# Kernel tuning notes

Measured on AMD Instinct MI355X. Metric: run time of the kernel, lower is better.

Reference implementation:

```python
import jax, jax.numpy as jnp
import numpy as np

T = 4096
V = 88   # visible_dim
H = 512  # hidden_dim
R = 512  # rnn_hidden_dim
REG_FACTOR = 0.2
GIBBS_STEPS = 20
EPS = 1e-6


def setup_inputs() -> dict:
    key = jax.random.key(0)
    ks = jax.random.split(key, 8)
    scale = 1.0 / np.sqrt(H)
    return {
        "visible": (jax.random.uniform(ks[0], (T, V)) < 0.5).astype(jnp.float32),
        "rand_h": jax.random.uniform(ks[1], (T - 1, GIBBS_STEPS, H), dtype=jnp.float32),
        "rand_v": jax.random.uniform(ks[2], (T - 1, GIBBS_STEPS, V), dtype=jnp.float32),
        "w": jax.random.normal(ks[3], (H, V), dtype=jnp.float32) * scale,
        "wuu": jax.random.normal(ks[4], (R, R), dtype=jnp.float32) * scale,
        "wuv": jax.random.normal(ks[5], (V, R), dtype=jnp.float32) * scale,
        "wuh": jax.random.normal(ks[6], (H, R), dtype=jnp.float32) * scale,
        "wvu": jax.random.normal(ks[7], (R, V), dtype=jnp.float32) * scale,
        "bv": jnp.zeros((V,), jnp.float32),
        "bh": jnp.zeros((H,), jnp.float32),
        "bu": jnp.zeros((R,), jnp.float32),
        "u0": jnp.zeros((R,), jnp.float32),
    }


def reference(visible, rand_h, rand_v, w, wuu, wuv, wuh, wvu, bv, bh, bu, u0):
    time_steps = visible.shape[0]
    v_seq = visible[1:]  # v_t for t = 1..T-1, shape [T-1, V]

    # RNN state depends only on data, not on Gibbs samples -> single scan.
    def u_step(u_prev, v_t):
        u_new = jnp.tanh(wvu @ v_t + wuu @ u_prev + bu)
        return u_new, u_prev  # emit u_{t-1} (bias conditioning state)

    _, u_prev = jax.lax.scan(u_step, u0, v_seq)  # [T-1, R]

    # Per-timestep RBM biases (F.linear(u, W, b) = u @ W.T + b).
    bh_t = u_prev @ wuh.T + bh  # [T-1, H]
    bv_t = u_prev @ wuv.T + bv  # [T-1, V]

    # 20 Gibbs steps, batched over all time steps at once.
    def gibbs_step(v, rands):
        rh, rv = rands  # [T-1, H], [T-1, V]
        p_h = jax.nn.sigmoid(v @ w.T + bh_t)
        h = jax.nn.relu(jnp.sign(p_h - rh))         # Bernoulli sample
        p_v = jax.nn.sigmoid(h @ w + bv_t)
        v_new = jax.nn.relu(jnp.sign(p_v - rv))
        return v_new, None

    neg, _ = jax.lax.scan(
        gibbs_step, v_seq,
        (jnp.swapaxes(rand_h, 0, 1), jnp.swapaxes(rand_v, 0, 1)),
    )  # negative samples [T-1, V]

    # Cross-entropy between data and sigmoid(bv_t), summed then /time_steps.
    y_t = jax.nn.sigmoid(bv_t)
    total_cost = jnp.sum(
        -v_seq * jnp.log(EPS + y_t) - (1.0 - v_seq) * jnp.log(EPS + 1.0 - y_t)
    ) / time_steps

    reg_term = (jnp.linalg.norm(wuv) + jnp.linalg.norm(wuh)) * REG_FACTOR
    total_cost = total_cost + reg_term

    mse = jnp.mean(jnp.abs(v_seq - neg), axis=1)  # per-timestep, [T-1]
    return total_cost, mse, reg_term
```

## Files before the change

### kernel.cpp

```cpp
#include <hip/hip_runtime.h>
#include <cstdint>
#include <cstddef>

#define T4096 4096
#define TM1 4095
#define NV 88
#define NH 512
#define NR 512
#define GS 20
#define EPSV 1e-6f

#define U_OFF 0
#define AB_OFF 2096640
#define BV_OFF 4193280
#define SC_OFF 4553640

__device__ __forceinline__ unsigned int agent_load_u32(const unsigned int* p) {
  return __hip_atomic_load(p, __ATOMIC_RELAXED, __HIP_MEMORY_SCOPE_AGENT);
}
__device__ __forceinline__ void agent_store_f32(float* p, float v) {
  __hip_atomic_store(p, v, __ATOMIC_RELAXED, __HIP_MEMORY_SCOPE_AGENT);
}
__device__ __forceinline__ float sigmoidf_(float x) {
  return 1.0f / (1.0f + expf(-x));
}

__device__ __forceinline__ void store_sc0(float* p, float v) {
  asm volatile("global_store_dword %0, %1, off sc0" :: "v"(p), "v"(v) : "memory");
}
__device__ __forceinline__ unsigned load_sc0(const unsigned* p) {
  unsigned r;
  asm volatile("global_load_dword %0, %1, off sc0\n\ts_waitcnt vmcnt(0)"
               : "=v"(r) : "v"(p) : "memory");
  return r;
}

__device__ __forceinline__ unsigned poll_nd_sc0(const unsigned* p,
                                                unsigned& s1, unsigned& s2,
                                                unsigned& s3, unsigned& s4) {
  unsigned rA;
  asm volatile(
    "v_mov_b32 %0, -1\n\t"
    "global_load_dword %1, %5, off sc0\n\t"
    "global_load_dword %2, %5, off sc0\n\t"
    "global_load_dword %3, %5, off sc0\n\t"
    "global_load_dword %4, %5, off sc0\n\t"
    "Lr%=:\n\t"
    "s_waitcnt vmcnt(3)\n\t"
    "v_cmp_ne_u32 vcc, -1, %1\n\t"
    "v_cndmask_b32 %0, %0, %1, vcc\n\t"
    "v_cmp_eq_u32 vcc, -1, %0\n\t"
    "s_cbranch_vccz Le%=\n\t"
    "global_load_dword %1, %5, off sc0\n\t"
    "s_waitcnt vmcnt(3)\n\t"
    "v_cmp_ne_u32 vcc, -1, %2\n\t"
    "v_cndmask_b32 %0, %0, %2, vcc\n\t"
    "v_cmp_eq_u32 vcc, -1, %0\n\t"
    "s_cbranch_vccz Le%=\n\t"
    "global_load_dword %2, %5, off sc0\n\t"
    "s_waitcnt vmcnt(3)\n\t"
    "v_cmp_ne_u32 vcc, -1, %3\n\t"
    "v_cndmask_b32 %0, %0, %3, vcc\n\t"
    "v_cmp_eq_u32 vcc, -1, %0\n\t"
    "s_cbranch_vccz Le%=\n\t"
    "global_load_dword %3, %5, off sc0\n\t"
    "s_waitcnt vmcnt(3)\n\t"
    "v_cmp_ne_u32 vcc, -1, %4\n\t"
    "v_cndmask_b32 %0, %0, %4, vcc\n\t"
    "v_cmp_eq_u32 vcc, -1, %0\n\t"
    "s_cbranch_vccz Le%=\n\t"
    "global_load_dword %4, %5, off sc0\n\t"
    "s_branch Lr%=\n\t"
    "Le%=:\n\t"
    : "=&v"(rA), "+v"(s1), "+v"(s2), "+v"(s3), "+v"(s4)
    : "v"(p) : "vcc", "memory");
  return rA;
}
__device__ __forceinline__ unsigned poll_nd_sys(const unsigned* p,
                                                unsigned& s1, unsigned& s2,
                                                unsigned& s3, unsigned& s4) {
  unsigned rA;
  asm volatile(
    "v_mov_b32 %0, -1\n\t"
    "global_load_dword %1, %5, off sc0 sc1\n\t"
    "global_load_dword %2, %5, off sc0 sc1\n\t"
    "global_load_dword %3, %5, off sc0 sc1\n\t"
    "global_load_dword %4, %5, off sc0 sc1\n\t"
    "Lq%=:\n\t"
    "s_waitcnt vmcnt(3)\n\t"
    "v_cmp_ne_u32 vcc, -1, %1\n\t"
    "v_cndmask_b32 %0, %0, %1, vcc\n\t"
    "v_cmp_eq_u32 vcc, -1, %0\n\t"
    "s_cbranch_vccz Lf%=\n\t"
    "global_load_dword %1, %5, off sc0 sc1\n\t"
    "s_waitcnt vmcnt(3)\n\t"
    "v_cmp_ne_u32 vcc, -1, %2\n\t"
    "v_cndmask_b32 %0, %0, %2, vcc\n\t"
    "v_cmp_eq_u32 vcc, -1, %0\n\t"
    "s_cbranch_vccz Lf%=\n\t"
    "global_load_dword %2, %5, off sc0 sc1\n\t"
    "s_waitcnt vmcnt(3)\n\t"
    "v_cmp_ne_u32 vcc, -1, %3\n\t"
    "v_cndmask_b32 %0, %0, %3, vcc\n\t"
    "v_cmp_eq_u32 vcc, -1, %0\n\t"
    "s_cbranch_vccz Lf%=\n\t"
    "global_load_dword %3, %5, off sc0 sc1\n\t"
    "s_waitcnt vmcnt(3)\n\t"
    "v_cmp_ne_u32 vcc, -1, %4\n\t"
    "v_cndmask_b32 %0, %0, %4, vcc\n\t"
    "v_cmp_eq_u32 vcc, -1, %0\n\t"
    "s_cbranch_vccz Lf%=\n\t"
    "global_load_dword %4, %5, off sc0 sc1\n\t"
    "s_branch Lq%=\n\t"
    "Lf%=:\n\t"
    : "=&v"(rA), "+v"(s1), "+v"(s2), "+v"(s3), "+v"(s4)
    : "v"(p) : "vcc", "memory");
  return rA;
}

__global__ __launch_bounds__(256) void k_a(const float* __restrict__ visible,
                                           const float* __restrict__ wvu,
                                           const float* __restrict__ bu,
                                           float* __restrict__ A) {
  __shared__ float vbuf[NV * 8];
  const int tid = threadIdx.x;
  const int t0 = blockIdx.x * 8;
  for (int idx = tid; idx < NV * 8; idx += 256) {
    int j = idx / NV, v = idx - j * NV;
    int t = t0 + j;
    vbuf[v * 8 + j] = (t < TM1) ? visible[(size_t)(t + 1) * NV + v] : 0.f;
  }
  __syncthreads();
  for (int rr = 0; rr < 2; rr++) {
    int r = tid + rr * 256;
    float b0 = bu[r];
    float acc[8];
#pragma unroll
    for (int j = 0; j < 8; j++) acc[j] = b0;
    const float* wr = wvu + (size_t)r * NV;
    for (int v = 0; v < NV; v++) {
      float wv = wr[v];
#pragma unroll
      for (int j = 0; j < 8; j++) acc[j] = fmaf(wv, vbuf[v * 8 + j], acc[j]);
    }
#pragma unroll
    for (int j = 0; j < 8; j++) {
      int t = t0 + j;
      if (t < TM1) A[(size_t)t * NR + r] = acc[j];
    }
  }
}

__global__ __launch_bounds__(256) void k_r(const float* __restrict__ wuv,
                                           const float* __restrict__ wuh,
                                           float* __restrict__ sc) {
  size_t stride = (size_t)gridDim.x * 256;
  size_t gid = (size_t)blockIdx.x * 256 + threadIdx.x;
  float s1 = 0.f, s2 = 0.f;
  for (size_t i = gid; i < (size_t)NV * NR; i += stride) { float x = wuv[i]; s1 = fmaf(x, x, s1); }
  for (size_t i = gid; i < (size_t)NH * NR; i += stride) { float x = wuh[i]; s2 = fmaf(x, x, s2); }
  for (int off = 32; off > 0; off >>= 1) {
    s1 += __shfl_down(s1, off, 64);
    s2 += __shfl_down(s2, off, 64);
  }
  if ((threadIdx.x & 63) == 0) {
    atomicAdd(&sc[1], s1);
    atomicAdd(&sc[2], s2);
  }
}

__global__ __launch_bounds__(512, 2) void k_u9(const float* __restrict__ wuu,
                                               const float* __restrict__ A,
                                               const float* __restrict__ u0,
                                               float* __restrict__ U,
                                               unsigned* __restrict__ ub) {
  __shared__ int s_slot;
  __shared__ int s_fast;
  __shared__ float u_buf[NR];
  __shared__ float partials[2][1024];
  const int tid = threadIdx.x;
  unsigned* claimc = ub + 8;
  unsigned* winner = ub + 16;
  unsigned* hs     = ub + 17;
  unsigned* vd     = ub + 33;

  if (tid == 0) {
    unsigned xcd;
    asm volatile("s_getreg_b32 %0, hwreg(HW_REG_XCC_ID, 0, 4)" : "=s"(xcd));
    xcd &= 7u;
    unsigned c = atomicAdd(&claimc[xcd], 1u);
    int slot = -1;
    if (c < 4u) {
      if (c == 3u) atomicCAS(winner, 0xFFFFFFFFu, xcd);
      unsigned wnr;
      do { wnr = agent_load_u32(winner); } while (wnr == 0xFFFFFFFFu);
      if (wnr == xcd) slot = (int)c;
    }
    s_slot = slot;
  }
  __syncthreads();
  const int slot = s_slot;
  if (slot < 0) return;

  if (tid == 0) {
    int fast = 1;
    for (int round = 0; round < 4 && fast; ++round) {
      unsigned* hw = hs + round * 4;
      store_sc0((float*)&hw[slot], 0.0f);
      for (int o = 0; o < 4; ++o) {
        if (o == slot) continue;
        int ok = 0;
        for (int it = 0; it < 300; ++it) {
          if (load_sc0(&hw[o]) != 0xFFFFFFFFu) { ok = 1; break; }
        }
        if (!ok) fast = 0;
      }
    }
    __hip_atomic_store(&vd[slot], (unsigned)(fast ? 1 : 0),
                       __ATOMIC_RELAXED, __HIP_MEMORY_SCOPE_AGENT);
    for (int o = 0; o < 4; ++o) {
      unsigned v;
      do { v = agent_load_u32(&vd[o]); } while (v == 0xFFFFFFFFu);
      if (v != 1u) fast = 0;
    }
    s_fast = fast;
  }
  __syncthreads();
  const int fast = s_fast;

  const int lane = tid & 63;
  const int kc   = tid >> 6;
  const int r0   = slot * 128;
  const bool is_red = (kc >> 1) == slot;
  const int s_row = ((kc & 1) << 6) + lane;
  float* ubw = u_buf + kc * 64;

  float WregA[64], WregB[64];
  {
    const float* wra = wuu + (size_t)(r0 + lane) * NR + kc * 64;
    const float* wrb = wuu + (size_t)(r0 + lane + 64) * NR + kc * 64;
#pragma unroll
    for (int i = 0; i < 16; i++) {
      ((float4*)WregA)[i] = ((const float4*)wra)[i];
      ((float4*)WregB)[i] = ((const float4*)wrb)[i];
    }
  }
#pragma unroll
  for (int i = 0; i < 64; i++) asm volatile("" : "+v"(WregA[i]));
#pragma unroll
  for (int i = 0; i < 64; i++) asm volatile("" : "+v"(WregB[i]));

  float val = 0.f, a_cur = 0.f;
  if (is_red) {
    agent_store_f32(&U[r0 + s_row], u0[r0 + s_row]);
    a_cur = A[r0 + s_row];
  }
  unsigned ps1 = 0, ps2 = 0, ps3 = 0, ps4 = 0;
  __syncthreads();

#define KU_STEP(T_, UVAL_) do {                                                \
    ubw[lane] = (UVAL_);                                                       \
    float acc0 = 0.f, acc1 = 0.f;                                              \
    _Pragma("unroll")                                                          \
    for (int i = 0; i < 64; i += 4) {                                          \
      float4 uv = *(const float4*)(ubw + i);                                   \
      acc0 = fmaf(WregA[i],     uv.x, acc0);                                   \
      acc1 = fmaf(WregB[i],     uv.x, acc1);                                   \
      acc0 = fmaf(WregA[i + 1], uv.y, acc0);                                   \
      acc1 = fmaf(WregB[i + 1], uv.y, acc1);                                   \
      acc0 = fmaf(WregA[i + 2], uv.z, acc0);                                   \
      acc1 = fmaf(WregB[i + 2], uv.z, acc1);                                   \
      acc0 = fmaf(WregA[i + 3], uv.w, acc0);                                   \
      acc1 = fmaf(WregB[i + 3], uv.w, acc1);                                   \
    }                                                                          \
    float* pb = partials[(T_) & 1];                                            \
    pb[kc * 128 + lane] = acc0;                                                \
    pb[kc * 128 + lane + 64] = acc1;                                           \
    __syncthreads();                                                           \
    if (is_red) {                                                              \
      float s = a_cur;                                                         \
      _Pragma("unroll")                                                        \
      for (int kk = 0; kk < 8; kk++) s += pb[kk * 128 + s_row];                \
      val = tanhf(s);                                                          \
      if (fast) store_sc0(&U[(size_t)(T_) * NR + r0 + s_row], val);            \
      else      agent_store_f32(&U[(size_t)(T_) * NR + r0 + s_row], val);      \
      a_cur = A[(size_t)(T_) * NR + r0 + s_row];    \
    }                                                                          \
  } while (0)

  KU_STEP(1, u0[kc * 64 + lane]);
  for (int t = 2; t <= TM1 - 1; t++) {
    float u_val;
    if (is_red) {
      u_val = val;
    } else {
      const unsigned* p = (const unsigned*)(U + (size_t)(t - 1) * NR) + kc * 64 + lane;
      unsigned w = fast ? poll_nd_sc0(p, ps1, ps2, ps3, ps4)
                        : poll_nd_sys(p, ps1, ps2, ps3, ps4);
      u_val = __uint_as_float(w);
    }
    KU_STEP(t, u_val);
  }
#undef KU_STEP
}

__global__ __launch_bounds__(256) void k_bh(const float* __restrict__ Uu,
                                            const float* __restrict__ wuh,
                                            const float* __restrict__ wuv,
                                            const float* __restrict__ bh,
                                            const float* __restrict__ bv,
                                            const float* __restrict__ visible,
                                            float* __restrict__ bht,
                                            float* __restrict__ bvt,
                                            float* __restrict__ sc) {
  __shared__ float uT[NR * 20];
  __shared__ float red[256];
  const int tid = threadIdx.x;
  const int t0 = blockIdx.x * 16;
  const int nt = min(16, TM1 - t0);
  for (int idx = tid; idx < 16 * NR; idx += 256) {
    int tt = idx >> 9, k = idx & 511;
    uT[k * 20 + tt] = (tt < nt) ? Uu[(size_t)(t0 + tt) * NR + k] : 0.f;
  }
  __syncthreads();
  const int h1 = tid, h2 = tid + 256;
  const bool hasv = tid < NV;
  float acc1[16], acc2[16], accv[16];
#pragma unroll
  for (int i = 0; i < 16; i++) acc1[i] = acc2[i] = accv[i] = 0.f;
  const float* w1p = wuh + (size_t)h1 * NR;
  const float* w2p = wuh + (size_t)h2 * NR;
  const float* wvp = wuv + (size_t)(hasv ? tid : 0) * NR;
  for (int k = 0; k < NR; k++) {
    float u16[16];
#pragma unroll
    for (int q = 0; q < 4; q++) *(float4*)(u16 + 4 * q) = *(const float4*)(uT + k * 20 + 4 * q);
    float a = w1p[k], b = w2p[k];
    float c = hasv ? wvp[k] : 0.f;
#pragma unroll
    for (int i = 0; i < 16; i++) {
      acc1[i] = fmaf(a, u16[i], acc1[i]);
      acc2[i] = fmaf(b, u16[i], acc2[i]);
      accv[i] = fmaf(c, u16[i], accv[i]);
    }
  }
  float bh1 = bh[h1], bh2 = bh[h2];
#pragma unroll
  for (int i = 0; i < 16; i++) {
    if (i < nt) {
      bht[(size_t)(t0 + i) * NH + h1] = acc1[i] + bh1;
      bht[(size_t)(t0 + i) * NH + h2] = acc2[i] + bh2;
    }
  }
  float ce = 0.f;
  if (hasv) {
    float bvv = bv[tid];
    for (int i = 0; i < nt; i++) {
      float x = accv[i] + bvv;
      bvt[(size_t)(t0 + i) * NV + tid] = x;
      float y = sigmoidf_(x);
      float vs = visible[(size_t)(t0 + i + 1) * NV + tid];
      ce += -vs * logf(EPSV + y) - (1.f - vs) * logf(EPSV + 1.f - y);
    }
  }
  red[tid] = ce;
  __syncthreads();
  for (int s = 128; s > 0; s >>= 1) {
    if (tid < s) red[tid] += red[tid + s];
    __syncthreads();
  }
  if (tid == 0) atomicAdd(&sc[0], red[0]);
}

__global__ __launch_bounds__(256) void k_g(const float* __restrict__ w,
                                           const float* __restrict__ visible,
                                           const float* __restrict__ rand_h,
                                           const float* __restrict__ rand_v,
                                           const float* __restrict__ bht,
                                           const float* __restrict__ bvt,
                                           float* __restrict__ out) {
  __shared__ float vlds[NV * 20];
  __shared__ float hlds[NH * 20];
  const int tid = threadIdx.x;
  const int t0 = blockIdx.x * 16;
  const int nt = min(16, TM1 - t0);
  for (int idx = tid; idx < NV * 16; idx += 256) {
    int j = idx / NV, v = idx - j * NV;
    vlds[v * 20 + j] = (j < nt) ? visible[(size_t)(t0 + j + 1) * NV + v] : 0.f;
  }
  for (int idx = tid; idx < NH * 20; idx += 256) hlds[idx] = 0.f;
  __syncthreads();
  const int h1 = tid, h2 = tid + 256;
  const int tg = tid >> 5, vg = tid & 31;
  const int v0 = vg * 4;
  const bool bact = vg < 22;
  for (int k = 0; k < GS; k++) {
    {
      float acc1[16], acc2[16];
#pragma unroll
      for (int i = 0; i < 16; i++) acc1[i] = acc2[i] = 0.f;
      const float* w1p = w + (size_t)h1 * NV;
      const float* w2p = w + (size_t)h2 * NV;
      for (int v = 0; v < NV; v++) {
        float vv[16];
#pragma unroll
        for (int q = 0; q < 4; q++) *(float4*)(vv + 4 * q) = *(const float4*)(vlds + v * 20 + 4 * q);
        float a = w1p[v], b = w2p[v];
#pragma unroll
        for (int i = 0; i < 16; i++) {
          acc1[i] = fmaf(a, vv[i], acc1[i]);
          acc2[i] = fmaf(b, vv[i], acc2[i]);
        }
      }
#pragma unroll
      for (int i = 0; i < 16; i++) {
        if (i < nt) {
          size_t t = (size_t)(t0 + i);
          float x1 = acc1[i] + bht[t * NH + h1];
          float x2 = acc2[i] + bht[t * NH + h2];
          float p1 = sigmoidf_(x1);
          float p2 = sigmoidf_(x2);
          float r1 = rand_h[(t * GS + k) * NH + h1];
          float r2 = rand_h[(t * GS + k) * NH + h2];
          hlds[h1 * 20 + i] = (p1 > r1) ? 1.f : 0.f;
          hlds[h2 * 20 + i] = (p2 > r2) ? 1.f : 0.f;
        }
      }
    }
    __syncthreads();
    if (bact) {
      float acc[2][4];
#pragma unroll
      for (int a = 0; a < 2; a++)
#pragma unroll
        for (int b = 0; b < 4; b++) acc[a][b] = 0.f;
#pragma unroll 4
      for (int h = 0; h < NH; h++) {
        float2 hv = *(const float2*)(hlds + h * 20 + tg * 2);
        float4 w4 = *(const float4*)(w + (size_t)h * NV + v0);
        acc[0][0] = fmaf(hv.x, w4.x, acc[0][0]);
        acc[0][1] = fmaf(hv.x, w4.y, acc[0][1]);
        acc[0][2] = fmaf(hv.x, w4.z, acc[0][2]);
        acc[0][3] = fmaf(hv.x, w4.w, acc[0][3]);
        acc[1][0] = fmaf(hv.y, w4.x, acc[1][0]);
        acc[1][1] = fmaf(hv.y, w4.y, acc[1][1]);
        acc[1][2] = fmaf(hv.y, w4.z, acc[1][2]);
        acc[1][3] = fmaf(hv.y, w4.w, acc[1][3]);
      }
#pragma unroll
      for (int a = 0; a < 2; a++) {
        int tt = tg * 2 + a;
        if (tt < nt) {
          size_t t = (size_t)(t0 + tt);
#pragma unroll
          for (int i = 0; i < 4; i++) {
            int v = v0 + i;
            float x = acc[a][i] + bvt[t * NV + v];
            float p = sigmoidf_(x);
            float r = rand_v[(t * GS + k) * NV + v];
            vlds[v * 20 + tt] = (p > r) ? 1.f : 0.f;
          }
        }
      }
    }
    __syncthreads();
  }
  if (tid < 16 && tid < nt) {
    int tt = tid;
    float s = 0.f;
    for (int v = 0; v < NV; v++) {
      float vs = visible[(size_t)(t0 + tt + 1) * NV + v];
      s += fabsf(vs - vlds[v * 20 + tt]);
    }
    out[1 + t0 + tt] = s / 88.f;
  }
}

__global__ void k_f(const float* __restrict__ sc, float* __restrict__ out) {
  float reg = 0.2f * (sqrtf(sc[1]) + sqrtf(sc[2]));
  out[0] = sc[0] / 4096.f + reg;
  out[4096] = reg;
}

extern "C" void kernel_launch(void* const* d_in, const int* in_sizes, int n_in,
                              void* d_out, int out_size, void* d_ws, size_t ws_size,
                              hipStream_t stream) {
  const float* visible = (const float*)d_in[0];
  const float* rand_h  = (const float*)d_in[1];
  const float* rand_v  = (const float*)d_in[2];
  const float* w       = (const float*)d_in[3];
  const float* wuu     = (const float*)d_in[4];
  const float* wuv     = (const float*)d_in[5];
  const float* wuh     = (const float*)d_in[6];
  const float* wvu     = (const float*)d_in[7];
  const float* bv      = (const float*)d_in[8];
  const float* bh      = (const float*)d_in[9];
  const float* bu      = (const float*)d_in[10];
  const float* u0      = (const float*)d_in[11];
  float* out = (float*)d_out;
  float* ws = (float*)d_ws;

  float* Uarr = ws + U_OFF;
  float* Aarr = ws + AB_OFF;
  float* bht  = ws + AB_OFF;
  float* bvt  = ws + BV_OFF;
  float* sc   = ws + SC_OFF;
  unsigned* ub = (unsigned*)sc;

  hipMemsetAsync(Uarr, 0xFF, (size_t)TM1 * NR * sizeof(float), stream);
  hipMemsetAsync(sc, 0, 64, stream);
  hipMemsetAsync((char*)sc + 64, 0xFF, 96, stream);

  k_a<<<512, 256, 0, stream>>>(visible, wvu, bu, Aarr);
  k_r<<<64, 256, 0, stream>>>(wuv, wuh, sc);
  k_u9<<<64, 512, 0, stream>>>(wuu, Aarr, u0, Uarr, ub);
  k_bh<<<256, 256, 0, stream>>>(Uarr, wuh, wuv, bh, bv, visible, bht, bvt, sc);
  k_g<<<256, 256, 0, stream>>>(w, visible, rand_h, rand_v, bht, bvt, out);
  k_f<<<1, 1, 0, stream>>>(sc, out);
}
```

Before: 5.512 ms.

## Fuse bias and Gibbs stages into recurrence kernel as flag-gated consumer blocks

The serial RNN recurrence kernel now runs alongside 256 consumer blocks in the same launch. Each consumer waits on per-slice progress flags that the recurrence blocks publish every 16 steps, then computes the per-timestep biases, the cross-entropy term and the 20 Gibbs steps for 8 timesteps at a time, keeping the biases in LDS. This overlaps the dependent bias and Gibbs work with the long sequential recurrence and removes the global bht/bvt round trip and two kernel launches. The cost is system-scope stores and loads, spin-wait polling, smaller per-block tiles, and reliance on all 260 blocks being co-resident to avoid deadlock.

```diff
diff --git a/kernel.cpp b/kernel.cpp
--- a/kernel.cpp
+++ b/kernel.cpp
@@ -33,6 +33,24 @@
   asm volatile("global_load_dword %0, %1, off sc0\n\ts_waitcnt vmcnt(0)"
                : "=v"(r) : "v"(p) : "memory");
   return r;
+}
+__device__ __forceinline__ void store_sys_f32(float* p, float v) {
+  asm volatile("global_store_dword %0, %1, off sc0 sc1" :: "v"(p), "v"(v) : "memory");
+}
+__device__ __forceinline__ void store_sys_u32(unsigned* p, unsigned v) {
+  asm volatile("global_store_dword %0, %1, off sc0 sc1" :: "v"(p), "v"(v) : "memory");
+}
+__device__ __forceinline__ unsigned load_sys_u32(const unsigned* p) {
+  unsigned r;
+  asm volatile("global_load_dword %0, %1, off sc0 sc1\n\ts_waitcnt vmcnt(0)"
+               : "=v"(r) : "v"(p) : "memory");
+  return r;
+}
+__device__ __forceinline__ float load_sys_f32(const float* p) {
+  unsigned r;
+  asm volatile("global_load_dword %0, %1, off sc0 sc1\n\ts_waitcnt vmcnt(0)"
+               : "=v"(r) : "v"(p) : "memory");
+  return __uint_as_float(r);
 }
 
 __device__ __forceinline__ unsigned poll_nd_sc0(const unsigned* p,
@@ -169,20 +187,35 @@
   }
 }
 
-__global__ __launch_bounds__(512, 2) void k_u9(const float* __restrict__ wuu,
-                                               const float* __restrict__ A,
-                                               const float* __restrict__ u0,
-                                               float* __restrict__ U,
-                                               unsigned* __restrict__ ub) {
+__global__ __launch_bounds__(512, 2) void k_u11(const float* __restrict__ wuu,
+                                                float* A,
+                                                const float* __restrict__ u0,
+                                                float* __restrict__ U,
+                                                unsigned* __restrict__ ub,
+                                                const float* __restrict__ visible,
+                                                const float* __restrict__ w,
+                                                const float* __restrict__ rand_h,
+                                                const float* __restrict__ rand_v,
+                                                const float* __restrict__ wuh,
+                                                const float* __restrict__ wuv,
+                                                const float* __restrict__ bh,
+                                                const float* __restrict__ bv,
+                                                float* __restrict__ out) {
   __shared__ int s_slot;
   __shared__ int s_fast;
-  __shared__ float u_buf[NR];
-  __shared__ float partials[2][1024];
+  __shared__ int s_cid;
+  __shared__ float red2[256];
+  __shared__ __align__(16) union {
+    struct { float u_buf[NR]; float partials[2][1024]; } p;
+    struct { float bht[8 * NH]; float bvt[8 * NV]; float uT[NR * 10]; } b;
+    struct { float bht[8 * NH]; float bvt[8 * NV]; float vlds[NV * 10]; float hlds[NH * 10]; } g;
+  } sh;
   const int tid = threadIdx.x;
   unsigned* claimc = ub + 8;
   unsigned* winner = ub + 16;
   unsigned* hs     = ub + 17;
   unsigned* vd     = ub + 33;
+  unsigned* flags  = ub + 40;
 
   if (tid == 0) {
     unsigned xcd;
@@ -200,7 +233,149 @@
   }
   __syncthreads();
   const int slot = s_slot;
-  if (slot < 0) return;
+
+  if (slot < 0) {
+    if (tid == 0) s_cid = (int)atomicAdd(&ub[48], 1u);
+    __syncthreads();
+    const int cid = s_cid;
+    if (cid >= 256) return;
+    float ce = 0.f;
+    for (int half = 0; half < 2; half++) {
+      const int c = cid * 2 + half;
+      const int t0 = c * 8;
+      const int nt = min(8, TM1 - t0);
+      unsigned need = (unsigned)((t0 + nt - 1 + 15) & ~15);
+      if (need > 4080u) need = 4095u;
+      if (tid == 0) {
+        for (;;) {
+          unsigned mn = 0xFFFFFFFFu;
+          for (int i = 0; i < 8; i++) { unsigned f = load_sys_u32(&flags[i]); if (f < mn) mn = f; }
+          if (mn >= need) break;
+          __builtin_amdgcn_s_sleep(32);
+        }
+      }
+      __syncthreads();
+      for (int idx = tid; idx < 8 * NR; idx += 512) {
+        int tt = idx >> 9, k = idx & 511;
+        int t = t0 + tt;
+        float v = 0.f;
+        if (tt < nt) v = (t == 0) ? u0[k] : load_sys_f32(&A[(size_t)(t - 1) * NR + k]);
+        sh.b.uT[k * 10 + tt] = v;
+      }
+      __syncthreads();
+      {
+        const int h = tid;
+        const bool hasv = tid < NV;
+        float acc1[8], accv[8];
+#pragma unroll
+        for (int i = 0; i < 8; i++) acc1[i] = accv[i] = 0.f;
+        const float* w1p = wuh + (size_t)h * NR;
+        const float* wvp = wuv + (size_t)(hasv ? tid : 0) * NR;
+        for (int k = 0; k < NR; k++) {
+          float u8[8];
+#pragma unroll
+          for (int q = 0; q < 2; q++) *(float4*)(u8 + 4 * q) = *(const float4*)(sh.b.uT + k * 10 + 4 * q);
+          float a = w1p[k];
+          float cc = hasv ? wvp[k] : 0.f;
+#pragma unroll
+          for (int i = 0; i < 8; i++) {
+            acc1[i] = fmaf(a, u8[i], acc1[i]);
+            accv[i] = fmaf(cc, u8[i], accv[i]);
+          }
+        }
+        float bh1 = bh[h];
+#pragma unroll
+        for (int i = 0; i < 8; i++)
+          if (i < nt) sh.b.bht[i * NH + h] = acc1[i] + bh1;
+        if (hasv) {
+          float bvv = bv[tid];
+          for (int i = 0; i < nt; i++) {
+            float x = accv[i] + bvv;
+            sh.b.bvt[i * NV + tid] = x;
+            float y = sigmoidf_(x);
+            float vs = visible[(size_t)(t0 + i + 1) * NV + tid];
+            ce += -vs * logf(EPSV + y) - (1.f - vs) * logf(EPSV + 1.f - y);
+          }
+        }
+      }
+      __syncthreads();
+      for (int idx = tid; idx < NV * 8; idx += 512) {
+        int j = idx / NV, v = idx - j * NV;
+        sh.g.vlds[v * 10 + j] = (j < nt) ? visible[(size_t)(t0 + j + 1) * NV + v] : 0.f;
+      }
+      __syncthreads();
+      const int h1 = tid;
+      const int tg = tid >> 5, vg = tid & 31;
+      const int v0 = vg * 4;
+      const bool bact = (vg < 22) && (tg < 8);
+      for (int k = 0; k < GS; k++) {
+        {
+          float acc1[8];
+#pragma unroll
+          for (int i = 0; i < 8; i++) acc1[i] = 0.f;
+          const float* w1p = w + (size_t)h1 * NV;
+          for (int v = 0; v < NV; v++) {
+            float vv[8];
+#pragma unroll
+            for (int q = 0; q < 2; q++) *(float4*)(vv + 4 * q) = *(const float4*)(sh.g.vlds + v * 10 + 4 * q);
+            float a = w1p[v];
+#pragma unroll
+            for (int i = 0; i < 8; i++) acc1[i] = fmaf(a, vv[i], acc1[i]);
+          }
+#pragma unroll
+          for (int i = 0; i < 8; i++) {
+            if (i < nt) {
+              size_t t = (size_t)(t0 + i);
+              float x1 = acc1[i] + sh.g.bht[i * NH + h1];
+              float p1 = sigmoidf_(x1);
+              float r1 = rand_h[(t * GS + k) * NH + h1];
+              sh.g.hlds[h1 * 10 + i] = (p1 > r1) ? 1.f : 0.f;
+            }
+          }
+        }
+        __syncthreads();
+        if (bact && tg < nt) {
+          float acc[4] = {0.f, 0.f, 0.f, 0.f};
+#pragma unroll 4
+          for (int h = 0; h < NH; h++) {
+            float hv = sh.g.hlds[h * 10 + tg];
+            float4 w4 = *(const float4*)(w + (size_t)h * NV + v0);
+            acc[0] = fmaf(hv, w4.x, acc[0]);
+            acc[1] = fmaf(hv, w4.y, acc[1]);
+            acc[2] = fmaf(hv, w4.z, acc[2]);
+            acc[3] = fmaf(hv, w4.w, acc[3]);
+          }
+          size_t t = (size_t)(t0 + tg);
+#pragma unroll
+          for (int i = 0; i < 4; i++) {
+            int v = v0 + i;
+            float x = acc[i] + sh.g.bvt[tg * NV + v];
+            float p = sigmoidf_(x);
+            float r = rand_v[(t * GS + k) * NV + v];
+            sh.g.vlds[v * 10 + tg] = (p > r) ? 1.f : 0.f;
+          }
+        }
+        __syncthreads();
+      }
+      if (tid < nt) {
+        float s = 0.f;
+        for (int v = 0; v < NV; v++) {
+          float vs = visible[(size_t)(t0 + tid + 1) * NV + v];
+          s += fabsf(vs - sh.g.vlds[v * 10 + tid]);
+        }
+        out[1 + t0 + tid] = s / 88.f;
+      }
+      __syncthreads();
+    }
+    if (tid < 256) red2[tid] = ce;
+    __syncthreads();
+    for (int s = 128; s > 0; s >>= 1) {
+      if (tid < s) red2[tid] += red2[tid + s];
+      __syncthreads();
+    }
+    if (tid == 0) atomicAdd((float*)ub, red2[0]);
+    return;
+  }
 
   if (tid == 0) {
     int fast = 1;
@@ -233,7 +408,8 @@
   const int r0   = slot * 128;
   const bool is_red = (kc >> 1) == slot;
   const int s_row = ((kc & 1) << 6) + lane;
-  float* ubw = u_buf + kc * 64;
+  const int fid = slot * 2 + (kc & 1);
+  float* ubw = sh.p.u_buf + kc * 64;
 
   float WregA[64], WregB[64];
   {
@@ -273,7 +449,7 @@
       acc0 = fmaf(WregA[i + 3], uv.w, acc0);                                   \
       acc1 = fmaf(WregB[i + 3], uv.w, acc1);                                   \
     }                                                                          \
-    float* pb = partials[(T_) & 1];                                            \
+    float* pb = sh.p.partials[(T_) & 1];                                       \
     pb[kc * 128 + lane] = acc0;                                                \
     pb[kc * 128 + lane + 64] = acc1;                                           \
     __syncthreads();                                                           \
@@ -284,7 +460,12 @@
       val = tanhf(s);                                                          \
       if (fast) store_sc0(&U[(size_t)(T_) * NR + r0 + s_row], val);            \
       else      agent_store_f32(&U[(size_t)(T_) * NR + r0 + s_row], val);      \
+      store_sys_f32(&A[(size_t)((T_) - 1) * NR + r0 + s_row], val);            \
       a_cur = A[(size_t)(T_) * NR + r0 + s_row];    \
+      if (((T_) & 15) == 0) {                                                  \
+        asm volatile("s_waitcnt vmcnt(0)" ::: "memory");                       \
+        if (lane == 0) store_sys_u32(&flags[fid], (unsigned)(T_));             \
+      }                                                                        \
     }                                                                          \
   } while (0)
 
@@ -295,184 +476,16 @@
       u_val = val;
     } else {
       const unsigned* p = (const unsigned*)(U + (size_t)(t - 1) * NR) + kc * 64 + lane;
-      unsigned w = fast ? poll_nd_sc0(p, ps1, ps2, ps3, ps4)
-                        : poll_nd_sys(p, ps1, ps2, ps3, ps4);
-      u_val = __uint_as_float(w);
+      unsigned wv = fast ? poll_nd_sc0(p, ps1, ps2, ps3, ps4)
+                         : poll_nd_sys(p, ps1, ps2, ps3, ps4);
+      u_val = __uint_as_float(wv);
     }
     KU_STEP(t, u_val);
   }
 #undef KU_STEP
-}
-
-__global__ __launch_bounds__(256) void k_bh(const float* __restrict__ Uu,
-                                            const float* __restrict__ wuh,
-                                            const float* __restrict__ wuv,
-                                            const float* __restrict__ bh,
-                                            const float* __restrict__ bv,
-                                            const float* __restrict__ visible,
-                                            float* __restrict__ bht,
-                                            float* __restrict__ bvt,
-                                            float* __restrict__ sc) {
-  __shared__ float uT[NR * 20];
-  __shared__ float red[256];
-  const int tid = threadIdx.x;
-  const int t0 = blockIdx.x * 16;
-  const int nt = min(16, TM1 - t0);
-  for (int idx = tid; idx < 16 * NR; idx += 256) {
-    int tt = idx >> 9, k = idx & 511;
-    uT[k * 20 + tt] = (tt < nt) ? Uu[(size_t)(t0 + tt) * NR + k] : 0.f;
-  }
-  __syncthreads();
-  const int h1 = tid, h2 = tid + 256;
-  const bool hasv = tid < NV;
-  float acc1[16], acc2[16], accv[16];
-#pragma unroll
-  for (int i = 0; i < 16; i++) acc1[i] = acc2[i] = accv[i] = 0.f;
-  const float* w1p = wuh + (size_t)h1 * NR;
-  const float* w2p = wuh + (size_t)h2 * NR;
-  const float* wvp = wuv + (size_t)(hasv ? tid : 0) * NR;
-  for (int k = 0; k < NR; k++) {
-    float u16[16];
-#pragma unroll
-    for (int q = 0; q < 4; q++) *(float4*)(u16 + 4 * q) = *(const float4*)(uT + k * 20 + 4 * q);
-    float a = w1p[k], b = w2p[k];
-    float c = hasv ? wvp[k] : 0.f;
-#pragma unroll
-    for (int i = 0; i < 16; i++) {
-      acc1[i] = fmaf(a, u16[i], acc1[i]);
-      acc2[i] = fmaf(b, u16[i], acc2[i]);
-      accv[i] = fmaf(c, u16[i], accv[i]);
-    }
-  }
-  float bh1 = bh[h1], bh2 = bh[h2];
-#pragma unroll
-  for (int i = 0; i < 16; i++) {
-    if (i < nt) {
-      bht[(size_t)(t0 + i) * NH + h1] = acc1[i] + bh1;
-      bht[(size_t)(t0 + i) * NH + h2] = acc2[i] + bh2;
-    }
-  }
-  float ce = 0.f;
-  if (hasv) {
-    float bvv = bv[tid];
-    for (int i = 0; i < nt; i++) {
-      float x = accv[i] + bvv;
-      bvt[(size_t)(t0 + i) * NV + tid] = x;
-      float y = sigmoidf_(x);
-      float vs = visible[(size_t)(t0 + i + 1) * NV + tid];
-      ce += -vs * logf(EPSV + y) - (1.f - vs) * logf(EPSV + 1.f - y);
-    }
-  }
-  red[tid] = ce;
-  __syncthreads();
-  for (int s = 128; s > 0; s >>= 1) {
-    if (tid < s) red[tid] += red[tid + s];
-    __syncthreads();
-  }
-  if (tid == 0) atomicAdd(&sc[0], red[0]);
-}
-
-__global__ __launch_bounds__(256) void k_g(const float* __restrict__ w,
-                                           const float* __restrict__ visible,
-                                           const float* __restrict__ rand_h,
-                                           const float* __restrict__ rand_v,
-                                           const float* __restrict__ bht,
-                                           const float* __restrict__ bvt,
-                                           float* __restrict__ out) {
-  __shared__ float vlds[NV * 20];
-  __shared__ float hlds[NH * 20];
-  const int tid = threadIdx.x;
-  const int t0 = blockIdx.x * 16;
-  const int nt = min(16, TM1 - t0);
-  for (int idx = tid; idx < NV * 16; idx += 256) {
-    int j = idx / NV, v = idx - j * NV;
-    vlds[v * 20 + j] = (j < nt) ? visible[(size_t)(t0 + j + 1) * NV + v] : 0.f;
-  }
-  for (int idx = tid; idx < NH * 20; idx += 256) hlds[idx] = 0.f;
-  __syncthreads();
-  const int h1 = tid, h2 = tid + 256;
-  const int tg = tid >> 5, vg = tid & 31;
-  const int v0 = vg * 4;
-  const bool bact = vg < 22;
-  for (int k = 0; k < GS; k++) {
-    {
-      float acc1[16], acc2[16];
-#pragma unroll
-      for (int i = 0; i < 16; i++) acc1[i] = acc2[i] = 0.f;
-      const float* w1p = w + (size_t)h1 * NV;
-      const float* w2p = w + (size_t)h2 * NV;
-      for (int v = 0; v < NV; v++) {
-        float vv[16];
-#pragma unroll
-        for (int q = 0; q < 4; q++) *(float4*)(vv + 4 * q) = *(const float4*)(vlds + v * 20 + 4 * q);
-        float a = w1p[v], b = w2p[v];
-#pragma unroll
-        for (int i = 0; i < 16; i++) {
-          acc1[i] = fmaf(a, vv[i], acc1[i]);
-          acc2[i] = fmaf(b, vv[i], acc2[i]);
-        }
-      }
-#pragma unroll
-      for (int i = 0; i < 16; i++) {
-        if (i < nt) {
-          size_t t = (size_t)(t0 + i);
-          float x1 = acc1[i] + bht[t * NH + h1];
-          float x2 = acc2[i] + bht[t * NH + h2];
-          float p1 = sigmoidf_(x1);
-          float p2 = sigmoidf_(x2);
-          float r1 = rand_h[(t * GS + k) * NH + h1];
-          float r2 = rand_h[(t * GS + k) * NH + h2];
-          hlds[h1 * 20 + i] = (p1 > r1) ? 1.f : 0.f;
-          hlds[h2 * 20 + i] = (p2 > r2) ? 1.f : 0.f;
-        }
-      }
-    }
-    __syncthreads();
-    if (bact) {
-      float acc[2][4];
-#pragma unroll
-      for (int a = 0; a < 2; a++)
-#pragma unroll
-        for (int b = 0; b < 4; b++) acc[a][b] = 0.f;
-#pragma unroll 4
-      for (int h = 0; h < NH; h++) {
-        float2 hv = *(const float2*)(hlds + h * 20 + tg * 2);
-        float4 w4 = *(const float4*)(w + (size_t)h * NV + v0);
-        acc[0][0] = fmaf(hv.x, w4.x, acc[0][0]);
-        acc[0][1] = fmaf(hv.x, w4.y, acc[0][1]);
-        acc[0][2] = fmaf(hv.x, w4.z, acc[0][2]);
-        acc[0][3] = fmaf(hv.x, w4.w, acc[0][3]);
-        acc[1][0] = fmaf(hv.y, w4.x, acc[1][0]);
-        acc[1][1] = fmaf(hv.y, w4.y, acc[1][1]);
-        acc[1][2] = fmaf(hv.y, w4.z, acc[1][2]);
-        acc[1][3] = fmaf(hv.y, w4.w, acc[1][3]);
-      }
-#pragma unroll
-      for (int a = 0; a < 2; a++) {
-        int tt = tg * 2 + a;
-        if (tt < nt) {
-          size_t t = (size_t)(t0 + tt);
-#pragma unroll
-          for (int i = 0; i < 4; i++) {
-            int v = v0 + i;
-            float x = acc[a][i] + bvt[t * NV + v];
-            float p = sigmoidf_(x);
-            float r = rand_v[(t * GS + k) * NV + v];
-            vlds[v * 20 + tt] = (p > r) ? 1.f : 0.f;
-          }
-        }
-      }
-    }
-    __syncthreads();
-  }
-  if (tid < 16 && tid < nt) {
-    int tt = tid;
-    float s = 0.f;
-    for (int v = 0; v < NV; v++) {
-      float vs = visible[(size_t)(t0 + tt + 1) * NV + v];
-      s += fabsf(vs - vlds[v * 20 + tt]);
-    }
-    out[1 + t0 + tt] = s / 88.f;
+  if (is_red) {
+    asm volatile("s_waitcnt vmcnt(0)" ::: "memory");
+    if (lane == 0) store_sys_u32(&flags[fid], 4095u);
   }
 }
 
@@ -502,19 +515,18 @@
 
   float* Uarr = ws + U_OFF;
   float* Aarr = ws + AB_OFF;
-  float* bht  = ws + AB_OFF;
-  float* bvt  = ws + BV_OFF;
   float* sc   = ws + SC_OFF;
   unsigned* ub = (unsigned*)sc;
 
   hipMemsetAsync(Uarr, 0xFF, (size_t)TM1 * NR * sizeof(float), stream);
   hipMemsetAsync(sc, 0, 64, stream);
   hipMemsetAsync((char*)sc + 64, 0xFF, 96, stream);
+  hipMemsetAsync((char*)sc + 160, 0, 64, stream);
 
   k_a<<<512, 256, 0, stream>>>(visible, wvu, bu, Aarr);
   k_r<<<64, 256, 0, stream>>>(wuv, wuh, sc);
-  k_u9<<<64, 512, 0, stream>>>(wuu, Aarr, u0, Uarr, ub);
-  k_bh<<<256, 256, 0, stream>>>(Uarr, wuh, wuv, bh, bv, visible, bht, bvt, sc);
-  k_g<<<256, 256, 0, stream>>>(w, visible, rand_h, rand_v, bht, bvt, out);
+  k_u11<<<260, 512, 0, stream>>>(wuu, Aarr, u0, Uarr, ub,
+                                 visible, w, rand_h, rand_v,
+                                 wuh, wuv, bh, bv, out);
   k_f<<<1, 1, 0, stream>>>(sc, out);
 }
```

Measured after the change: 5.777 ms. +4.8%, slower.
